# Kernel optimization log

Hardware: AMD Instinct MI355X
Metric: run time of the kernel (lower is better)

The kernel has to match this reference:

```python
import jax, jax.numpy as jnp
import numpy as np

BN_EPS = 1e-5

def relu6(v):
    return jnp.clip(v, 0.0, 6.0)

def setup_inputs() -> dict:
    key = jax.random.key(0)
    ks = jax.random.split(key, 7)
    C, R = 512, 128  # in_channels, reduced_channels = C // 4
    B, H, W = 8, 128, 128
    x = jax.random.normal(ks[0], (B, C, H, W), dtype=jnp.float32)
    # 1x1 convs stored as [out_ch, in_ch] matrices (kernel is 1x1, no bias)
    w_guide = jax.random.normal(ks[1], (R, C), dtype=jnp.float32) * (1.0 / np.sqrt(C))
    w_fuse = jax.random.normal(ks[2], (C, R), dtype=jnp.float32) * (1.0 / np.sqrt(R))
    bn_gamma = jax.random.normal(ks[3], (C,), dtype=jnp.float32) * 0.1 + 1.0
    bn_beta = jax.random.normal(ks[4], (C,), dtype=jnp.float32) * 0.1
    bn_mean = jax.random.normal(ks[5], (C,), dtype=jnp.float32) * 0.1
    bn_var = jax.random.uniform(ks[6], (C,), dtype=jnp.float32, minval=0.5, maxval=1.5)
    return {"x": x, "w_guide": w_guide, "w_fuse": w_fuse,
            "bn_gamma": bn_gamma, "bn_beta": bn_beta,
            "bn_mean": bn_mean, "bn_var": bn_var}

def reference(x, w_guide, w_fuse, bn_gamma, bn_beta, bn_mean, bn_var):
    # y = AdaptiveAvgPool2d(1)(x): [B, C]
    y = jnp.mean(x, axis=(2, 3))
    # conv_guide: 1x1 conv (no bias) + ReLU6 on the 1x1 map -> [B, R]
    y = relu6(jnp.einsum('rc,bc->br', w_guide, y))
    # Nearest upsample of a 1x1 map then pointwise conv+BN+ReLU6 commutes:
    # compute conv_fuse once per (b, channel), then broadcast over H, W.
    y = jnp.einsum('cr,br->bc', w_fuse, y)  # 1x1 conv, no bias -> [B, C]
    inv_std = jax.lax.rsqrt(bn_var + BN_EPS)
    y = relu6((y - bn_mean) * inv_std * bn_gamma + bn_beta)
    # residual add with nearest-broadcast of the constant spatial map
    return x + y[:, :, None, None]
```

## Files before the change

### kernel.cpp

```cpp
#include <hip/hip_runtime.h>

#define C_CH  512
#define R_CH  128
#define BATCH 8
#define HW    16384
#define HW4   (HW / 4)
#define NPLANE (BATCH * C_CH)

__device__ __forceinline__ float relu6f(float v) {
    return fminf(fmaxf(v, 0.0f), 6.0f);
}

__global__ __launch_bounds__(256) void mean_kernel(const float4* __restrict__ x,
                                                   float* __restrict__ meanv) {
    const int plane = blockIdx.x;
    const float4* px = x + (size_t)plane * HW4;
    float s = 0.0f;
#pragma unroll
    for (int it = 0; it < HW4 / 256; ++it) {
        float4 v = px[threadIdx.x + it * 256];
        s += (v.x + v.y) + (v.z + v.w);
    }
    __shared__ float red[256];
    red[threadIdx.x] = s;
    __syncthreads();
    for (int off = 128; off > 0; off >>= 1) {
        if (threadIdx.x < off) red[threadIdx.x] += red[threadIdx.x + off];
        __syncthreads();
    }
    if (threadIdx.x == 0) meanv[plane] = red[0] * (1.0f / (float)HW);
}

__global__ __launch_bounds__(256) void mlp_kernel(
    const float* __restrict__ meanv,
    const float* __restrict__ wg,
    const float* __restrict__ wf,
    const float* __restrict__ gamma,
    const float* __restrict__ beta,
    const float* __restrict__ mu,
    const float* __restrict__ var,
    float* __restrict__ yv) {
    const int b = blockIdx.x;
    __shared__ float m[C_CH];
    __shared__ float t[R_CH];
    for (int c = threadIdx.x; c < C_CH; c += 256) m[c] = meanv[b * C_CH + c];
    __syncthreads();
    if (threadIdx.x < R_CH) {
        const int r = threadIdx.x;
        const float4* w4 = (const float4*)(wg + (size_t)r * C_CH);
        float a0 = 0.f, a1 = 0.f;
#pragma unroll 8
        for (int i = 0; i < C_CH / 4; ++i) {
            float4 v = w4[i];
            const int c = i * 4;
            a0 += v.x * m[c + 0] + v.y * m[c + 1];
            a1 += v.z * m[c + 2] + v.w * m[c + 3];
        }
        t[r] = relu6f(a0 + a1);
    }
    __syncthreads();
    for (int c = threadIdx.x; c < C_CH; c += 256) {
        const float4* w4 = (const float4*)(wf + (size_t)c * R_CH);
        float a0 = 0.f, a1 = 0.f;
#pragma unroll
        for (int i = 0; i < R_CH / 4; ++i) {
            float4 v = w4[i];
            const int r = i * 4;
            a0 += v.x * t[r + 0] + v.y * t[r + 1];
            a1 += v.z * t[r + 2] + v.w * t[r + 3];
        }
        const float s = a0 + a1;
        const float inv_std = 1.0f / sqrtf(var[c] + 1e-5f);
        const float v2 = (s - mu[c]) * inv_std * gamma[c] + beta[c];
        yv[b * C_CH + c] = relu6f(v2);
    }
}

__global__ __launch_bounds__(256) void add_kernel(const float4* __restrict__ x,
                                                  const float* __restrict__ yv,
                                                  float4* __restrict__ out) {
    const int plane = blockIdx.x;
    const float a = yv[plane];
    const float4* px = x + (size_t)plane * HW4;
    float4* po = out + (size_t)plane * HW4;
#pragma unroll
    for (int it = 0; it < HW4 / 256; ++it) {
        const int i = threadIdx.x + it * 256;
        float4 v = px[i];
        v.x += a; v.y += a; v.z += a; v.w += a;
        po[i] = v;
    }
}

extern "C" void kernel_launch(void* const* d_in, const int* in_sizes, int n_in,
                              void* d_out, int out_size, void* d_ws, size_t ws_size,
                              hipStream_t stream) {
    const float4* x4  = (const float4*)d_in[0];
    const float* wg   = (const float*)d_in[1];
    const float* wf   = (const float*)d_in[2];
    const float* gamma = (const float*)d_in[3];
    const float* beta  = (const float*)d_in[4];
    const float* mu    = (const float*)d_in[5];
    const float* var   = (const float*)d_in[6];

    float* meanv = (float*)d_ws;
    float* yv    = meanv + NPLANE;
    float4* out  = (float4*)d_out;

    mean_kernel<<<NPLANE, 256, 0, stream>>>(x4, meanv);
    mlp_kernel<<<BATCH, 256, 0, stream>>>(meanv, wg, wf, gamma, beta, mu, var, yv);
    add_kernel<<<NPLANE, 256, 0, stream>>>(x4, yv, out);
}
```

Baseline: 524.4 us.

## Fuse MLP into residual add kernel with reversed plane order and nontemporal stores

Merges the small per-batch MLP kernel and the broadcast-add kernel into one kernel. Each block redundantly recomputes the guide projection for its batch, then computes the fuse output for its 4 planes and adds it to them. Blocks run in reverse plane order so the most recently read (likely cache-resident) planes from the mean pass are reused first, and output uses nontemporal stores. The cost is redundant guide matvec work per block (1024 blocks each reading the 256KB w_guide), in exchange for removing one launch and the serial 8-block MLP stage.

Measured after the change: 509.1 us. 2.9% less time.

```diff
diff --git a/kernel.cpp b/kernel.cpp
--- a/kernel.cpp
+++ b/kernel.cpp
@@ -6,6 +6,10 @@
 #define HW    16384
 #define HW4   (HW / 4)
 #define NPLANE (BATCH * C_CH)
+#define PPB   4
+#define NBLK  (NPLANE / PPB)
+
+typedef float floatx4 __attribute__((ext_vector_type(4)));
 
 __device__ __forceinline__ float relu6f(float v) {
     return fminf(fmaxf(v, 0.0f), 6.0f);
@@ -31,7 +35,8 @@
     if (threadIdx.x == 0) meanv[plane] = red[0] * (1.0f / (float)HW);
 }
 
-__global__ __launch_bounds__(256) void mlp_kernel(
+__global__ __launch_bounds__(256) void fused_kernel(
+    const float4* __restrict__ x,
     const float* __restrict__ meanv,
     const float* __restrict__ wg,
     const float* __restrict__ wf,
@@ -39,27 +44,42 @@
     const float* __restrict__ beta,
     const float* __restrict__ mu,
     const float* __restrict__ var,
-    float* __restrict__ yv) {
-    const int b = blockIdx.x;
+    float4* __restrict__ out) {
+    const int g = (NBLK - 1) - (int)blockIdx.x;
+    const int plane0 = g * PPB;
+    const int b = plane0 >> 9;
+    const int c0 = plane0 & (C_CH - 1);
+
     __shared__ float m[C_CH];
+    __shared__ float part[256];
     __shared__ float t[R_CH];
-    for (int c = threadIdx.x; c < C_CH; c += 256) m[c] = meanv[b * C_CH + c];
+    __shared__ float yv[PPB];
+
+    const int tid = threadIdx.x;
+    for (int c = tid; c < C_CH; c += 256) m[c] = meanv[b * C_CH + c];
     __syncthreads();
-    if (threadIdx.x < R_CH) {
-        const int r = threadIdx.x;
-        const float4* w4 = (const float4*)(wg + (size_t)r * C_CH);
+
+    {
+        const int r = tid & (R_CH - 1);
+        const int half = tid >> 7;
+        const float4* w4 = (const float4*)(wg + (size_t)r * C_CH) + half * (C_CH / 8);
+        const float* mh = m + half * (C_CH / 2);
         float a0 = 0.f, a1 = 0.f;
 #pragma unroll 8
-        for (int i = 0; i < C_CH / 4; ++i) {
+        for (int i = 0; i < C_CH / 8; ++i) {
             float4 v = w4[i];
             const int c = i * 4;
-            a0 += v.x * m[c + 0] + v.y * m[c + 1];
-            a1 += v.z * m[c + 2] + v.w * m[c + 3];
+            a0 += v.x * mh[c + 0] + v.y * mh[c + 1];
+            a1 += v.z * mh[c + 2] + v.w * mh[c + 3];
         }
-        t[r] = relu6f(a0 + a1);
+        part[tid] = a0 + a1;
     }
     __syncthreads();
-    for (int c = threadIdx.x; c < C_CH; c += 256) {
+    if (tid < R_CH) t[tid] = relu6f(part[tid] + part[tid + R_CH]);
+    __syncthreads();
+
+    if (tid < PPB) {
+        const int c = c0 + tid;
         const float4* w4 = (const float4*)(wf + (size_t)c * R_CH);
         float a0 = 0.f, a1 = 0.f;
 #pragma unroll
@@ -71,24 +91,23 @@
         }
         const float s = a0 + a1;
         const float inv_std = 1.0f / sqrtf(var[c] + 1e-5f);
-        const float v2 = (s - mu[c]) * inv_std * gamma[c] + beta[c];
-        yv[b * C_CH + c] = relu6f(v2);
+        yv[tid] = relu6f((s - mu[c]) * inv_std * gamma[c] + beta[c]);
     }
-}
+    __syncthreads();
 
-__global__ __launch_bounds__(256) void add_kernel(const float4* __restrict__ x,
-                                                  const float* __restrict__ yv,
-                                                  float4* __restrict__ out) {
-    const int plane = blockIdx.x;
-    const float a = yv[plane];
-    const float4* px = x + (size_t)plane * HW4;
-    float4* po = out + (size_t)plane * HW4;
 #pragma unroll
-    for (int it = 0; it < HW4 / 256; ++it) {
-        const int i = threadIdx.x + it * 256;
-        float4 v = px[i];
-        v.x += a; v.y += a; v.z += a; v.w += a;
-        po[i] = v;
+    for (int p = 0; p < PPB; ++p) {
+        const float a = yv[p];
+        const float4* px = x + (size_t)(plane0 + p) * HW4;
+        floatx4* po = reinterpret_cast<floatx4*>(out + (size_t)(plane0 + p) * HW4);
+#pragma unroll
+        for (int it = 0; it < HW4 / 256; ++it) {
+            const int i = tid + it * 256;
+            float4 v = px[i];
+            floatx4 w;
+            w.x = v.x + a; w.y = v.y + a; w.z = v.z + a; w.w = v.w + a;
+            __builtin_nontemporal_store(w, po + i);
+        }
     }
 }
 
@@ -104,10 +123,9 @@
     const float* var   = (const float*)d_in[6];
 
     float* meanv = (float*)d_ws;
-    float* yv    = meanv + NPLANE;
     float4* out  = (float4*)d_out;
 
     mean_kernel<<<NPLANE, 256, 0, stream>>>(x4, meanv);
-    mlp_kernel<<<BATCH, 256, 0, stream>>>(meanv, wg, wf, gamma, beta, mu, var, yv);
-    add_kernel<<<NPLANE, 256, 0, stream>>>(x4, yv, out);
+    fused_kernel<<<NBLK, 256, 0, stream>>>(x4, meanv, wg, wf, gamma, beta,
+                                           mu, var, out);
 }
```

## Fuse mean, MLP and add into one persistent kernel with grid barriers

Applied to the files above, without the earlier changes.

Replaces the three kernels with a single persistent kernel of 256 blocks. Each block keeps two channel planes for a pair of batches in registers, computes their means, syncs the whole grid through atomic barriers, recomputes the small MLP redundantly per block, and writes x plus the offset with nontemporal stores. The aim is to read x once instead of twice and to drop the extra launches. In exchange it depends on all 256 blocks being co-resident for the spin barriers, holds a large register array per thread, repeats the MLP work in every block, and adds a memset before each launch.

New measurement: 622.3 us. 18.7% more time.

```diff
diff --git a/kernel.cpp b/kernel.cpp
--- a/kernel.cpp
+++ b/kernel.cpp
@@ -5,109 +5,189 @@
 #define BATCH 8
 #define HW    16384
 #define HW4   (HW / 4)
-#define NPLANE (BATCH * C_CH)
+#define TPB   512
+#define NBLK  256
+#define F4PT  16
+
+typedef float floatx4 __attribute__((ext_vector_type(4)));
 
 __device__ __forceinline__ float relu6f(float v) {
     return fminf(fmaxf(v, 0.0f), 6.0f);
 }
 
-__global__ __launch_bounds__(256) void mean_kernel(const float4* __restrict__ x,
-                                                   float* __restrict__ meanv) {
-    const int plane = blockIdx.x;
-    const float4* px = x + (size_t)plane * HW4;
-    float s = 0.0f;
-#pragma unroll
-    for (int it = 0; it < HW4 / 256; ++it) {
-        float4 v = px[threadIdx.x + it * 256];
-        s += (v.x + v.y) + (v.z + v.w);
-    }
-    __shared__ float red[256];
-    red[threadIdx.x] = s;
-    __syncthreads();
-    for (int off = 128; off > 0; off >>= 1) {
-        if (threadIdx.x < off) red[threadIdx.x] += red[threadIdx.x + off];
-        __syncthreads();
-    }
-    if (threadIdx.x == 0) meanv[plane] = red[0] * (1.0f / (float)HW);
-}
-
-__global__ __launch_bounds__(256) void mlp_kernel(
-    const float* __restrict__ meanv,
+__global__ __launch_bounds__(TPB, 2) void fused_all(
+    const float4* __restrict__ x,
     const float* __restrict__ wg,
     const float* __restrict__ wf,
     const float* __restrict__ gamma,
     const float* __restrict__ beta,
     const float* __restrict__ mu,
     const float* __restrict__ var,
-    float* __restrict__ yv) {
-    const int b = blockIdx.x;
-    __shared__ float m[C_CH];
-    __shared__ float t[R_CH];
-    for (int c = threadIdx.x; c < C_CH; c += 256) m[c] = meanv[b * C_CH + c];
-    __syncthreads();
-    if (threadIdx.x < R_CH) {
-        const int r = threadIdx.x;
-        const float4* w4 = (const float4*)(wg + (size_t)r * C_CH);
-        float a0 = 0.f, a1 = 0.f;
-#pragma unroll 8
-        for (int i = 0; i < C_CH / 4; ++i) {
-            float4 v = w4[i];
-            const int c = i * 4;
-            a0 += v.x * m[c + 0] + v.y * m[c + 1];
-            a1 += v.z * m[c + 2] + v.w * m[c + 3];
+    float* __restrict__ meanv,
+    unsigned* __restrict__ bar,
+    floatx4* __restrict__ out)
+{
+    const int tid  = threadIdx.x;
+    const int half = tid >> 8;
+    const int t2   = tid & 255;
+    const int c    = 2 * (int)blockIdx.x + half;
+
+    __shared__ float red[2][2][256];
+    __shared__ float part[2][TPB];
+    __shared__ float m0[C_CH], m1[C_CH];
+    __shared__ float ts[2][R_CH];
+    __shared__ float ys[2][2];
+
+    float4 A[F4PT], B[F4PT];
+
+#define LOAD_AND_MEAN(B0, B1)                                                 \
+    {                                                                          \
+        const float4* pa = x + ((size_t)((B0) * C_CH + c)) * HW4;              \
+        const float4* pb = x + ((size_t)((B1) * C_CH + c)) * HW4;              \
+        _Pragma("unroll")                                                      \
+        for (int k = 0; k < F4PT; ++k) A[k] = pa[t2 + k * 256];                \
+        _Pragma("unroll")                                                      \
+        for (int k = 0; k < F4PT; ++k) B[k] = pb[t2 + k * 256];                \
+        float sA = 0.f, sB = 0.f;                                              \
+        _Pragma("unroll")                                                      \
+        for (int k = 0; k < F4PT; ++k) sA += (A[k].x + A[k].y) + (A[k].z + A[k].w); \
+        _Pragma("unroll")                                                      \
+        for (int k = 0; k < F4PT; ++k) sB += (B[k].x + B[k].y) + (B[k].z + B[k].w); \
+        red[half][0][t2] = sA; red[half][1][t2] = sB;                          \
+        __syncthreads();                                                       \
+        for (int off = 128; off > 0; off >>= 1) {                              \
+            if (t2 < off) {                                                    \
+                red[half][0][t2] += red[half][0][t2 + off];                    \
+                red[half][1][t2] += red[half][1][t2 + off];                    \
+            }                                                                  \
+            __syncthreads();                                                   \
+        }                                                                      \
+        if (t2 == 0) {                                                         \
+            meanv[(B0) * C_CH + c] = red[half][0][0] * (1.0f / (float)HW);     \
+            meanv[(B1) * C_CH + c] = red[half][1][0] * (1.0f / (float)HW);     \
+        }                                                                      \
+    }
+
+#define GRID_BARRIER(J)                                                        \
+    {                                                                          \
+        __syncthreads();     \
+        if (tid == 0) {                                                        \
+            __threadfence();                        \
+            atomicAdd(&bar[(J)], 1u);                \
+            while (__hip_atomic_load(&bar[(J)], __ATOMIC_RELAXED,              \
+                                     __HIP_MEMORY_SCOPE_AGENT) < NBLK)         \
+                __builtin_amdgcn_s_sleep(2);                                   \
+            __threadfence();                          \
+        }                                                                      \
+        __syncthreads();                                                       \
+    }
+
+    LOAD_AND_MEAN(0, 1)
+    GRID_BARRIER(0)
+
+    for (int j = 0; j < 4; ++j) {
+        const int b0 = 2 * j, b1 = b0 + 1;
+
+        for (int k = tid; k < C_CH; k += TPB) {
+            m0[k] = __hip_atomic_load(&meanv[b0 * C_CH + k], __ATOMIC_RELAXED,
+                                      __HIP_MEMORY_SCOPE_AGENT);
+            m1[k] = __hip_atomic_load(&meanv[b1 * C_CH + k], __ATOMIC_RELAXED,
+                                      __HIP_MEMORY_SCOPE_AGENT);
         }
-        t[r] = relu6f(a0 + a1);
+        __syncthreads();
+
+        {
+            const int r = tid & (R_CH - 1);
+            const int q = tid >> 7;
+            const float4* w4 = (const float4*)(wg + (size_t)r * C_CH) + q * (C_CH / 16);
+            const float* mh0 = m0 + q * (C_CH / 4);
+            const float* mh1 = m1 + q * (C_CH / 4);
+            float a0 = 0.f, a1 = 0.f;
+#pragma unroll
+            for (int i = 0; i < C_CH / 16; ++i) {
+                float4 v = w4[i];
+                const int k4 = i * 4;
+                a0 += v.x * mh0[k4] + v.y * mh0[k4 + 1] + v.z * mh0[k4 + 2] + v.w * mh0[k4 + 3];
+                a1 += v.x * mh1[k4] + v.y * mh1[k4 + 1] + v.z * mh1[k4 + 2] + v.w * mh1[k4 + 3];
+            }
+            part[0][tid] = a0; part[1][tid] = a1;
+        }
+        __syncthreads();
+        if (tid < R_CH) {
+            ts[0][tid] = relu6f(part[0][tid] + part[0][tid + 128] +
+                                part[0][tid + 256] + part[0][tid + 384]);
+        } else if (tid < 2 * R_CH) {
+            const int r = tid - R_CH;
+            ts[1][r] = relu6f(part[1][r] + part[1][r + 128] +
+                              part[1][r + 256] + part[1][r + 384]);
+        }
+        __syncthreads();
+
+        if (tid < 128) {
+            const int ch = tid >> 6;
+            const int l  = tid & 63;
+            const int cc = 2 * (int)blockIdx.x + ch;
+            const float2 w2 = ((const float2*)(wf + (size_t)cc * R_CH))[l];
+            float s0 = w2.x * ts[0][2 * l] + w2.y * ts[0][2 * l + 1];
+            float s1 = w2.x * ts[1][2 * l] + w2.y * ts[1][2 * l + 1];
+            for (int off = 32; off > 0; off >>= 1) {
+                s0 += __shfl_down(s0, off);
+                s1 += __shfl_down(s1, off);
+            }
+            if (l == 0) {
+                const float is = 1.0f / sqrtf(var[cc] + 1e-5f);
+                const float sc = gamma[cc] * is;
+                const float bi = beta[cc] - mu[cc] * sc;
+                ys[ch][0] = relu6f(s0 * sc + bi);
+                ys[ch][1] = relu6f(s1 * sc + bi);
+            }
+        }
+        __syncthreads();
+        const float y0 = ys[half][0];
+        const float y1 = ys[half][1];
+
+        {
+            floatx4* po0 = out + ((size_t)(b0 * C_CH + c)) * HW4;
+            floatx4* po1 = out + ((size_t)(b1 * C_CH + c)) * HW4;
+#pragma unroll
+            for (int k = 0; k < F4PT; ++k) {
+                floatx4 w;
+                w.x = A[k].x + y0; w.y = A[k].y + y0; w.z = A[k].z + y0; w.w = A[k].w + y0;
+                __builtin_nontemporal_store(w, po0 + t2 + k * 256);
+            }
+#pragma unroll
+            for (int k = 0; k < F4PT; ++k) {
+                floatx4 w;
+                w.x = B[k].x + y1; w.y = B[k].y + y1; w.z = B[k].z + y1; w.w = B[k].w + y1;
+                __builtin_nontemporal_store(w, po1 + t2 + k * 256);
+            }
+        }
+
+        if (j < 3) {
+            LOAD_AND_MEAN(b0 + 2, b1 + 2)
+            GRID_BARRIER(j + 1)
+        }
     }
-    __syncthreads();
-    for (int c = threadIdx.x; c < C_CH; c += 256) {
-        const float4* w4 = (const float4*)(wf + (size_t)c * R_CH);
-        float a0 = 0.f, a1 = 0.f;
-#pragma unroll
-        for (int i = 0; i < R_CH / 4; ++i) {
-            float4 v = w4[i];
-            const int r = i * 4;
-            a0 += v.x * t[r + 0] + v.y * t[r + 1];
-            a1 += v.z * t[r + 2] + v.w * t[r + 3];
-        }
-        const float s = a0 + a1;
-        const float inv_std = 1.0f / sqrtf(var[c] + 1e-5f);
-        const float v2 = (s - mu[c]) * inv_std * gamma[c] + beta[c];
-        yv[b * C_CH + c] = relu6f(v2);
-    }
-}
-
-__global__ __launch_bounds__(256) void add_kernel(const float4* __restrict__ x,
-                                                  const float* __restrict__ yv,
-                                                  float4* __restrict__ out) {
-    const int plane = blockIdx.x;
-    const float a = yv[plane];
-    const float4* px = x + (size_t)plane * HW4;
-    float4* po = out + (size_t)plane * HW4;
-#pragma unroll
-    for (int it = 0; it < HW4 / 256; ++it) {
-        const int i = threadIdx.x + it * 256;
-        float4 v = px[i];
-        v.x += a; v.y += a; v.z += a; v.w += a;
-        po[i] = v;
-    }
+#undef LOAD_AND_MEAN
+#undef GRID_BARRIER
 }
 
 extern "C" void kernel_launch(void* const* d_in, const int* in_sizes, int n_in,
                               void* d_out, int out_size, void* d_ws, size_t ws_size,
                               hipStream_t stream) {
-    const float4* x4  = (const float4*)d_in[0];
-    const float* wg   = (const float*)d_in[1];
-    const float* wf   = (const float*)d_in[2];
+    const float4* x4   = (const float4*)d_in[0];
+    const float* wg    = (const float*)d_in[1];
+    const float* wf    = (const float*)d_in[2];
     const float* gamma = (const float*)d_in[3];
     const float* beta  = (const float*)d_in[4];
     const float* mu    = (const float*)d_in[5];
     const float* var   = (const float*)d_in[6];
 
-    float* meanv = (float*)d_ws;
-    float* yv    = meanv + NPLANE;
-    float4* out  = (float4*)d_out;
+    unsigned* bar = (unsigned*)d_ws;
+    float* meanv  = (float*)d_ws + 64;
+    floatx4* out  = (floatx4*)d_out;
 
-    mean_kernel<<<NPLANE, 256, 0, stream>>>(x4, meanv);
-    mlp_kernel<<<BATCH, 256, 0, stream>>>(meanv, wg, wf, gamma, beta, mu, var, yv);
-    add_kernel<<<NPLANE, 256, 0, stream>>>(x4, yv, out);
+    hipMemsetAsync(d_ws, 0, 64, stream);
+    fused_all<<<NBLK, TPB, 0, stream>>>(x4, wg, wf, gamma, beta, mu, var,
+                                        meanv, bar, out);
 }
```
